# Kernel optimization log

Measured on AMD Instinct MI355X. Metric: run time of the kernel, lower is better.

Reference implementation:

```python
import jax, jax.numpy as jnp
import numpy as np

B, S, HIDDEN = 1, 2048, 2048
NUM_HEADS, MLA_DIM = 16, 128
HEAD_DIM = HIDDEN // NUM_HEADS
ROPE_BASE = 10000.0


def setup_inputs() -> dict:
    key = jax.random.key(0)
    ks = jax.random.split(key, 5)
    sd = 0.02
    hidden_states = jax.random.normal(ks[0], (B, S, HIDDEN), dtype=jnp.float32)
    wq = jax.random.normal(ks[1], (HIDDEN, NUM_HEADS * MLA_DIM), dtype=jnp.float32) * sd
    wk = jax.random.normal(ks[2], (HIDDEN, NUM_HEADS * MLA_DIM), dtype=jnp.float32) * sd
    wv = jax.random.normal(ks[3], (HIDDEN, HIDDEN), dtype=jnp.float32) * sd
    wo = jax.random.normal(ks[4], (HIDDEN, HIDDEN), dtype=jnp.float32) * sd
    # causal additive mask [B, 1, S, S]
    causal = jnp.tril(jnp.ones((S, S), dtype=bool))
    attention_mask = jnp.where(causal, 0.0, -1e9).astype(jnp.float32)[None, None]
    attention_mask = jnp.broadcast_to(attention_mask, (B, 1, S, S))
    return {"hidden_states": hidden_states, "wq": wq, "wk": wk, "wv": wv,
            "wo": wo, "attention_mask": attention_mask}


def _rope_cos_sin(seq_len, dim, dtype):
    inv_freq = 1.0 / (ROPE_BASE ** (jnp.arange(0, dim, 2, dtype=jnp.float32) / dim))
    t = jnp.arange(seq_len, dtype=jnp.float32)
    freqs = jnp.einsum('i,j->ij', t, inv_freq)           # [S, dim/2]
    emb = jnp.concatenate([freqs, freqs], axis=-1)       # [S, dim]
    cos = jnp.cos(emb)[None, :, None, :].astype(dtype)   # [1, S, 1, dim]
    sin = jnp.sin(emb)[None, :, None, :].astype(dtype)
    return cos, sin


def _rotate_half(x):
    x1, x2 = jnp.split(x, 2, axis=-1)
    return jnp.concatenate([-x2, x1], axis=-1)


def reference(hidden_states, wq, wk, wv, wo, attention_mask):
    b, s, _ = hidden_states.shape
    q = (hidden_states @ wq).reshape(b, s, NUM_HEADS, MLA_DIM)
    k = (hidden_states @ wk).reshape(b, s, NUM_HEADS, MLA_DIM)
    v = (hidden_states @ wv).reshape(b, s, NUM_HEADS, HEAD_DIM)
    cos, sin = _rope_cos_sin(s, MLA_DIM, q.dtype)
    q = q * cos + _rotate_half(q) * sin
    k = k * cos + _rotate_half(k) * sin
    scale = 1.0 / np.sqrt(MLA_DIM)
    scores = jnp.einsum('bqhd,bkhd->bhqk', q, k) * scale + attention_mask
    probs = jax.nn.softmax(scores, axis=-1)
    out = jnp.einsum('bhqk,bkhd->bqhd', probs, v).reshape(b, s, HIDDEN)
    return out @ wo
```

## Files before the change

### kernel.cpp

```cpp
#include <hip/hip_runtime.h>
#include <math.h>

namespace {

constexpr int SEQ = 2048;
constexpr int HID = 2048;
constexpr int NH  = 16;
constexpr int DH  = 128;

using f32x4  = __attribute__((ext_vector_type(4))) float;
using short8 = __attribute__((ext_vector_type(8))) short;

__device__ __forceinline__ unsigned short f2bf(float f) {
    unsigned u = __float_as_uint(f);
    u += 0x7FFFu + ((u >> 16) & 1u);
    return (unsigned short)(u >> 16);
}

typedef const __attribute__((address_space(1))) unsigned int GUI;
typedef __attribute__((address_space(3))) unsigned int LUI;
__device__ __forceinline__ void async16(const void* g, void* l) {
    __builtin_amdgcn_global_load_lds((GUI*)g, (LUI*)l, 16, 0, 0);
}

__global__ __launch_bounds__(256)
void cast_bf16(const float* __restrict__ X, unsigned short* __restrict__ Y)
{
    const int i = blockIdx.x * 256 + threadIdx.x;
    const float4 v = reinterpret_cast<const float4*>(X)[i];
    ushort4 o;
    o.x = f2bf(v.x); o.y = f2bf(v.y); o.z = f2bf(v.z); o.w = f2bf(v.w);
    reinterpret_cast<ushort4*>(Y)[i] = o;
}

__global__ __launch_bounds__(256)
void transpose_cast3(const float* __restrict__ w0, const float* __restrict__ w1,
                     const float* __restrict__ w2, unsigned short* __restrict__ WT3)
{
    const int z = blockIdx.z;
    const float* W = (z == 0) ? w0 : (z == 1) ? w1 : w2;
    unsigned short* WT = WT3 + (size_t)z * HID * HID;

    __shared__ float t[32][33];
    const int tx = threadIdx.x & 31, ty = threadIdx.x >> 5;
    const int n0 = blockIdx.x * 32, k0 = blockIdx.y * 32;
    #pragma unroll
    for (int i = 0; i < 4; ++i)
        t[ty + 8 * i][tx] = W[(size_t)(k0 + ty + 8 * i) * HID + n0 + tx];
    __syncthreads();
    #pragma unroll
    for (int i = 0; i < 4; ++i)
        WT[(size_t)(n0 + ty + 8 * i) * HID + k0 + tx] = f2bf(t[tx][ty + 8 * i]);
}

__global__ __launch_bounds__(256)
void transpose_cast(const float* __restrict__ W, unsigned short* __restrict__ WT)
{
    __shared__ float t[32][33];
    const int tx = threadIdx.x & 31, ty = threadIdx.x >> 5;
    const int n0 = blockIdx.x * 32, k0 = blockIdx.y * 32;
    #pragma unroll
    for (int i = 0; i < 4; ++i)
        t[ty + 8 * i][tx] = W[(size_t)(k0 + ty + 8 * i) * HID + n0 + tx];
    __syncthreads();
    #pragma unroll
    for (int i = 0; i < 4; ++i)
        WT[(size_t)(n0 + ty + 8 * i) * HID + k0 + tx] = f2bf(t[tx][ty + 8 * i]);
}

__global__ __launch_bounds__(256)
void transp_bf16(const unsigned short* __restrict__ X, unsigned short* __restrict__ Y)
{
    __shared__ unsigned short t[32][34];
    const int tx = threadIdx.x & 31, ty = threadIdx.x >> 5;
    const int i0 = blockIdx.y * 32, j0 = blockIdx.x * 32;
    #pragma unroll
    for (int q = 0; q < 4; ++q)
        t[ty + 8 * q][tx] = X[(size_t)(i0 + ty + 8 * q) * HID + j0 + tx];
    __syncthreads();
    #pragma unroll
    for (int q = 0; q < 4; ++q)
        Y[(size_t)(j0 + ty + 8 * q) * HID + i0 + tx] = t[tx][ty + 8 * q];
}

__global__ __launch_bounds__(256)
void gemm_qkv(const unsigned short* __restrict__ A,
              const unsigned short* __restrict__ Bt3,
              unsigned short* __restrict__ Qo,
              unsigned short* __restrict__ Ko,
              unsigned short* __restrict__ Vo)
{
    __shared__ unsigned short As[128 * 32];
    __shared__ unsigned short Bs[128 * 32];

    const int tid  = threadIdx.x;
    const int lane = tid & 63;
    const int w    = tid >> 6;
    const int wr   = w >> 1, wc = w & 1;

    const int b  = blockIdx.x;
    const int sw = (b & 7) * 96 + (b >> 3);
    const int mt = sw & 15, nt = sw >> 4;
    const int m0  = mt * 128;
    const int n0g = nt * 128;
    const int wi  = nt >> 4;
    const int n0  = (nt & 15) * 128;
    unsigned short* C = (wi == 0) ? Qo : (wi == 1) ? Ko : Vo;

    const int srow = lane >> 2;
    const int scol = (lane & 3) * 8;
    const int c0   = w * 2;

    const unsigned short* gA = A   + (size_t)(m0  + c0 * 16 + srow) * HID + scol;
    const unsigned short* gB = Bt3 + (size_t)(n0g + c0 * 16 + srow) * HID + scol;
    unsigned short* lA = &As[c0 * 16 * 32];
    unsigned short* lB = &Bs[c0 * 16 * 32];

    f32x4 acc[4][4] = {};

    for (int k0 = 0; k0 < HID; k0 += 32) {
        __syncthreads();
        async16(gA + k0,            lA);
        async16(gA + 16 * HID + k0, lA + 16 * 32);
        async16(gB + k0,            lB);
        async16(gB + 16 * HID + k0, lB + 16 * 32);
        __syncthreads();

        short8 af[4], bf[4];
        const int kb = (lane >> 4) * 8;
        #pragma unroll
        for (int i = 0; i < 4; ++i) {
            af[i] = *reinterpret_cast<const short8*>(
                &As[(wr * 64 + i * 16 + (lane & 15)) * 32 + kb]);
            bf[i] = *reinterpret_cast<const short8*>(
                &Bs[(wc * 64 + i * 16 + (lane & 15)) * 32 + kb]);
        }
        #pragma unroll
        for (int i = 0; i < 4; ++i)
            #pragma unroll
            for (int j = 0; j < 4; ++j)
                acc[i][j] = __builtin_amdgcn_mfma_f32_16x16x32_bf16(
                    af[i], bf[j], acc[i][j], 0, 0, 0);
    }

    const int cl = lane & 15, rg = (lane >> 4) * 4;
    #pragma unroll
    for (int i = 0; i < 4; ++i)
        #pragma unroll
        for (int j = 0; j < 4; ++j)
            #pragma unroll
            for (int rr = 0; rr < 4; ++rr) {
                const int row = m0 + wr * 64 + i * 16 + rg + rr;
                const int col = n0 + wc * 64 + j * 16 + cl;
                C[(size_t)row * HID + col] = f2bf(acc[i][j][rr]);
            }
}

__global__ __launch_bounds__(256)
void gemm_wo(const unsigned short* __restrict__ A,
             const unsigned short* __restrict__ Bt,
             float* __restrict__ C)
{
    __shared__ unsigned short As[128 * 32];
    __shared__ unsigned short Bs[128 * 32];

    const int tid  = threadIdx.x;
    const int lane = tid & 63;
    const int w    = tid >> 6;
    const int wr   = w >> 1, wc = w & 1;

    const int b  = blockIdx.x;
    const int sw = (b & 7) * 32 + (b >> 3);
    const int m0 = (sw >> 4) * 128, n0 = (sw & 15) * 128;

    const int srow = lane >> 2;
    const int scol = (lane & 3) * 8;
    const int c0   = w * 2;

    const unsigned short* gA = A  + (size_t)(m0 + c0 * 16 + srow) * HID + scol;
    const unsigned short* gB = Bt + (size_t)(n0 + c0 * 16 + srow) * HID + scol;
    unsigned short* lA = &As[c0 * 16 * 32];
    unsigned short* lB = &Bs[c0 * 16 * 32];

    f32x4 acc[4][4] = {};

    for (int k0 = 0; k0 < HID; k0 += 32) {
        __syncthreads();
        async16(gA + k0,            lA);
        async16(gA + 16 * HID + k0, lA + 16 * 32);
        async16(gB + k0,            lB);
        async16(gB + 16 * HID + k0, lB + 16 * 32);
        __syncthreads();

        short8 af[4], bf[4];
        const int kb = (lane >> 4) * 8;
        #pragma unroll
        for (int i = 0; i < 4; ++i) {
            af[i] = *reinterpret_cast<const short8*>(
                &As[(wr * 64 + i * 16 + (lane & 15)) * 32 + kb]);
            bf[i] = *reinterpret_cast<const short8*>(
                &Bs[(wc * 64 + i * 16 + (lane & 15)) * 32 + kb]);
        }
        #pragma unroll
        for (int i = 0; i < 4; ++i)
            #pragma unroll
            for (int j = 0; j < 4; ++j)
                acc[i][j] = __builtin_amdgcn_mfma_f32_16x16x32_bf16(
                    af[i], bf[j], acc[i][j], 0, 0, 0);
    }

    const int cl = lane & 15, rg = (lane >> 4) * 4;
    #pragma unroll
    for (int i = 0; i < 4; ++i)
        #pragma unroll
        for (int j = 0; j < 4; ++j)
            #pragma unroll
            for (int rr = 0; rr < 4; ++rr) {
                const int row = m0 + wr * 64 + i * 16 + rg + rr;
                const int col = n0 + wc * 64 + j * 16 + cl;
                C[(size_t)row * HID + col] = acc[i][j][rr];
            }
}

__global__ __launch_bounds__(256)
void rope_qk(unsigned short* __restrict__ Q, unsigned short* __restrict__ K)
{
    const int idx = blockIdx.x * 256 + threadIdx.x;
    const int d = idx & 63;
    const int h = (idx >> 6) & (NH - 1);
    const int s = idx >> 10;

    const float invf = exp2f(-(float)d * (13.287712379549449f / 64.0f));
    float sn, c;
    sincosf((float)s * invf, &sn, &c);

    const float SC = 0.08838834764831845f;
    const size_t base = (size_t)s * HID + h * DH + d;

    const float a0 = __uint_as_float((unsigned)Q[base]      << 16);
    const float a1 = __uint_as_float((unsigned)Q[base + 64] << 16);
    Q[base]      = f2bf((a0 * c - a1 * sn) * SC);
    Q[base + 64] = f2bf((a1 * c + a0 * sn) * SC);
    const float b0 = __uint_as_float((unsigned)K[base]      << 16);
    const float b1 = __uint_as_float((unsigned)K[base + 64] << 16);
    K[base]      = f2bf(b0 * c - b1 * sn);
    K[base + 64] = f2bf(b1 * c + b0 * sn);
}

__global__ __launch_bounds__(256)
void attn_mfma(const unsigned short* __restrict__ Q,
               const unsigned short* __restrict__ K,
               const unsigned short* __restrict__ Vt,
               unsigned short* __restrict__ AO)
{
    __shared__ unsigned short Ks[64 * 128];
    __shared__ unsigned short Vs[128 * 64];
    __shared__ unsigned short Ps[4][16 * 72];

    const int tid  = threadIdx.x;
    const int lane = tid & 63;
    const int w    = tid >> 6;

    const int b  = blockIdx.x;
    const int i_ = b & 31;
    const int h  = b >> 5;
    const int qb = (b < 256) ? i_ : 31 - i_;
    const int q0 = qb * 64;

    const int cl = lane & 15;
    const int lg = lane >> 4;
    const int rg = lg * 4;

    short8 aq[4];
    const unsigned short* qrow = Q + (size_t)(q0 + w * 16 + cl) * HID + h * DH;
    #pragma unroll
    for (int c = 0; c < 4; ++c)
        aq[c] = *reinterpret_cast<const short8*>(qrow + c * 32 + lg * 8);

    f32x4 o[8] = {};
    float m[4] = {-INFINITY, -INFINITY, -INFINITY, -INFINITY};
    float l[4] = {};

    const int nt = qb + 1;
    for (int t = 0; t < nt; ++t) {
        const int k0 = t * 64;

        __syncthreads();
        #pragma unroll
        for (int i = 0; i < 4; ++i) {
            const int rb = i * 16 + w * 4;
            const int r  = rb + lg;
            const int gs = cl ^ (r & 7);
            async16(K + (size_t)(k0 + r) * HID + h * DH + gs * 8, &Ks[rb * 128]);
        }
        #pragma unroll
        for (int i = 0; i < 4; ++i) {
            const int rb = i * 32 + w * 8;
            const int r  = rb + (lane >> 3);
            const int gs = (lane & 7) ^ (r & 7);
            async16(Vt + (size_t)(h * DH + r) * SEQ + k0 + gs * 8, &Vs[rb * 64]);
        }
        __syncthreads();

        f32x4 s4[4] = {};
        #pragma unroll
        for (int jk = 0; jk < 4; ++jk) {
            #pragma unroll
            for (int c = 0; c < 4; ++c) {
                const int row  = jk * 16 + cl;
                const int slot = (c * 4 + lg) ^ (row & 7);
                const short8 bk = *reinterpret_cast<const short8*>(
                    &Ks[row * 128 + slot * 8]);
                s4[jk] = __builtin_amdgcn_mfma_f32_16x16x32_bf16(
                    aq[c], bk, s4[jk], 0, 0, 0);
            }
        }

        if (t == nt - 1) {
            #pragma unroll
            for (int jk = 0; jk < 4; ++jk)
                #pragma unroll
                for (int r = 0; r < 4; ++r)
                    if (jk * 16 + cl > w * 16 + rg + r)
                        s4[jk][r] = -INFINITY;
        }

        float corr[4], rs[4];
        #pragma unroll
        for (int r = 0; r < 4; ++r) {
            float mx = fmaxf(fmaxf(s4[0][r], s4[1][r]),
                             fmaxf(s4[2][r], s4[3][r]));
            #pragma unroll
            for (int off = 1; off < 16; off <<= 1)
                mx = fmaxf(mx, __shfl_xor(mx, off, 64));
            const float mn = fmaxf(m[r], mx);
            corr[r] = __expf(m[r] - mn);
            m[r] = mn;
            rs[r] = 0.0f;
        }
        #pragma unroll
        for (int jk = 0; jk < 4; ++jk)
            #pragma unroll
            for (int r = 0; r < 4; ++r) {
                const float p = __expf(s4[jk][r] - m[r]);
                Ps[w][(rg + r) * 72 + jk * 16 + cl] = f2bf(p);
                rs[r] += p;
            }
        #pragma unroll
        for (int r = 0; r < 4; ++r) {
            #pragma unroll
            for (int off = 1; off < 16; off <<= 1)
                rs[r] += __shfl_xor(rs[r], off, 64);
            l[r] = l[r] * corr[r] + rs[r];
        }
        #pragma unroll
        for (int jd = 0; jd < 8; ++jd)
            #pragma unroll
            for (int r = 0; r < 4; ++r)
                o[jd][r] *= corr[r];

        #pragma unroll
        for (int c = 0; c < 2; ++c) {
            const short8 pa = *reinterpret_cast<const short8*>(
                &Ps[w][cl * 72 + c * 32 + lg * 8]);
            #pragma unroll
            for (int jd = 0; jd < 8; ++jd) {
                const int row  = jd * 16 + cl;
                const int slot = (c * 4 + lg) ^ (row & 7);
                const short8 bv = *reinterpret_cast<const short8*>(
                    &Vs[row * 64 + slot * 8]);
                o[jd] = __builtin_amdgcn_mfma_f32_16x16x32_bf16(
                    pa, bv, o[jd], 0, 0, 0);
            }
        }
    }

    #pragma unroll
    for (int r = 0; r < 4; ++r) {
        const float inv = 1.0f / l[r];
        unsigned short* orow = AO + (size_t)(q0 + w * 16 + rg + r) * HID + h * DH;
        #pragma unroll
        for (int jd = 0; jd < 8; ++jd)
            orow[jd * 16 + cl] = f2bf(o[jd][r] * inv);
    }
}

}

extern "C" void kernel_launch(void* const* d_in, const int* in_sizes, int n_in,
                              void* d_out, int out_size, void* d_ws, size_t ws_size,
                              hipStream_t stream)
{
    (void)in_sizes; (void)n_in; (void)out_size; (void)ws_size;

    const float* hs = (const float*)d_in[0];
    const float* wq = (const float*)d_in[1];
    const float* wk = (const float*)d_in[2];
    const float* wv = (const float*)d_in[3];
    const float* wo = (const float*)d_in[4];
    float* out = (float*)d_out;

    const size_t NE = (size_t)SEQ * HID;
    unsigned short* hsb = (unsigned short*)d_ws;
    unsigned short* Qb  = hsb + NE;
    unsigned short* Kb  = Qb + NE;
    unsigned short* Vb  = Kb + NE;
    unsigned short* WT3 = Vb + NE;
    unsigned short* AOb = WT3 + NE;
    unsigned short* WTo = WT3;
    unsigned short* Vt  = hsb;

    const dim3 tgrid(HID / 32, HID / 32);

    cast_bf16<<<(NE / 4) / 256, 256, 0, stream>>>(hs, hsb);

    transpose_cast3<<<dim3(HID / 32, HID / 32, 3), 256, 0, stream>>>(wq, wk, wv, WT3);

    gemm_qkv<<<768, 256, 0, stream>>>(hsb, WT3, Qb, Kb, Vb);

    rope_qk<<<(SEQ * NH * 64) / 256, 256, 0, stream>>>(Qb, Kb);

    transp_bf16<<<tgrid, 256, 0, stream>>>(Vb, Vt);

    attn_mfma<<<512, 256, 0, stream>>>(Qb, Kb, Vt, AOb);

    transpose_cast<<<tgrid, 256, 0, stream>>>(wo, WTo);
    gemm_wo<<<256, 256, 0, stream>>>(AOb, WTo, out);
}
```

Measured before the change: 319.6 us.

## Double-buffer attention K/V tiles, split-K the output GEMM, widen weight transposes

The attention kernel now double-buffers its K and V shared-memory tiles, so the next tile's async loads are issued while the current tile is computed, with one barrier per iteration. The output projection GEMM is split into two K-halves across 512 blocks, writing partial sums into reused workspace that a new reduce kernel adds together. This targets the GPU being under-filled when there was only one block per tile. The weight transpose-cast kernels now handle 64-column tiles with float2 loads. The costs are double the attention LDS footprint, an extra fp32 read/write pass plus a launch for the reduction, and reliance on workspace aliasing being safe.

```diff
diff --git a/kernel.cpp b/kernel.cpp
--- a/kernel.cpp
+++ b/kernel.cpp
@@ -41,31 +41,45 @@
     const float* W = (z == 0) ? w0 : (z == 1) ? w1 : w2;
     unsigned short* WT = WT3 + (size_t)z * HID * HID;
 
-    __shared__ float t[32][33];
+    __shared__ float t[32][66];
     const int tx = threadIdx.x & 31, ty = threadIdx.x >> 5;
-    const int n0 = blockIdx.x * 32, k0 = blockIdx.y * 32;
-    #pragma unroll
-    for (int i = 0; i < 4; ++i)
-        t[ty + 8 * i][tx] = W[(size_t)(k0 + ty + 8 * i) * HID + n0 + tx];
+    const int n0 = blockIdx.x * 64, k0 = blockIdx.y * 32;
+    #pragma unroll
+    for (int i = 0; i < 4; ++i) {
+        const int kr = ty + 8 * i;
+        const float2 v = *reinterpret_cast<const float2*>(
+            &W[(size_t)(k0 + kr) * HID + n0 + 2 * tx]);
+        t[kr][2 * tx]     = v.x;
+        t[kr][2 * tx + 1] = v.y;
+    }
     __syncthreads();
     #pragma unroll
-    for (int i = 0; i < 4; ++i)
-        WT[(size_t)(n0 + ty + 8 * i) * HID + k0 + tx] = f2bf(t[tx][ty + 8 * i]);
+    for (int i = 0; i < 8; ++i) {
+        const int n = ty + 8 * i;
+        WT[(size_t)(n0 + n) * HID + k0 + tx] = f2bf(t[tx][n]);
+    }
 }
 
 __global__ __launch_bounds__(256)
 void transpose_cast(const float* __restrict__ W, unsigned short* __restrict__ WT)
 {
-    __shared__ float t[32][33];
+    __shared__ float t[32][66];
     const int tx = threadIdx.x & 31, ty = threadIdx.x >> 5;
-    const int n0 = blockIdx.x * 32, k0 = blockIdx.y * 32;
-    #pragma unroll
-    for (int i = 0; i < 4; ++i)
-        t[ty + 8 * i][tx] = W[(size_t)(k0 + ty + 8 * i) * HID + n0 + tx];
+    const int n0 = blockIdx.x * 64, k0 = blockIdx.y * 32;
+    #pragma unroll
+    for (int i = 0; i < 4; ++i) {
+        const int kr = ty + 8 * i;
+        const float2 v = *reinterpret_cast<const float2*>(
+            &W[(size_t)(k0 + kr) * HID + n0 + 2 * tx]);
+        t[kr][2 * tx]     = v.x;
+        t[kr][2 * tx + 1] = v.y;
+    }
     __syncthreads();
     #pragma unroll
-    for (int i = 0; i < 4; ++i)
-        WT[(size_t)(n0 + ty + 8 * i) * HID + k0 + tx] = f2bf(t[tx][ty + 8 * i]);
+    for (int i = 0; i < 8; ++i) {
+        const int n = ty + 8 * i;
+        WT[(size_t)(n0 + n) * HID + k0 + tx] = f2bf(t[tx][n]);
+    }
 }
 
 __global__ __launch_bounds__(256)
@@ -157,9 +171,9 @@
 }
 
 __global__ __launch_bounds__(256)
-void gemm_wo(const unsigned short* __restrict__ A,
-             const unsigned short* __restrict__ Bt,
-             float* __restrict__ C)
+void gemm_wo_sk(const unsigned short* __restrict__ A,
+                const unsigned short* __restrict__ Bt,
+                float* __restrict__ P0, float* __restrict__ P1)
 {
     __shared__ unsigned short As[128 * 32];
     __shared__ unsigned short Bs[128 * 32];
@@ -169,22 +183,26 @@
     const int w    = tid >> 6;
     const int wr   = w >> 1, wc = w & 1;
 
-    const int b  = blockIdx.x;
-    const int sw = (b & 7) * 32 + (b >> 3);
+    const int b     = blockIdx.x;
+    const int chunk = b >> 8;
+    const int bb    = b & 255;
+    const int sw = (bb & 7) * 32 + (bb >> 3);
     const int m0 = (sw >> 4) * 128, n0 = (sw & 15) * 128;
+    float* C = chunk ? P1 : P0;
+    const int kbase = chunk * 1024;
 
     const int srow = lane >> 2;
     const int scol = (lane & 3) * 8;
     const int c0   = w * 2;
 
-    const unsigned short* gA = A  + (size_t)(m0 + c0 * 16 + srow) * HID + scol;
-    const unsigned short* gB = Bt + (size_t)(n0 + c0 * 16 + srow) * HID + scol;
+    const unsigned short* gA = A  + (size_t)(m0 + c0 * 16 + srow) * HID + kbase + scol;
+    const unsigned short* gB = Bt + (size_t)(n0 + c0 * 16 + srow) * HID + kbase + scol;
     unsigned short* lA = &As[c0 * 16 * 32];
     unsigned short* lB = &Bs[c0 * 16 * 32];
 
     f32x4 acc[4][4] = {};
 
-    for (int k0 = 0; k0 < HID; k0 += 32) {
+    for (int k0 = 0; k0 < 1024; k0 += 32) {
         __syncthreads();
         async16(gA + k0,            lA);
         async16(gA + 16 * HID + k0, lA + 16 * 32);
@@ -220,6 +238,17 @@
                 const int col = n0 + wc * 64 + j * 16 + cl;
                 C[(size_t)row * HID + col] = acc[i][j][rr];
             }
+}
+
+__global__ __launch_bounds__(256)
+void reduce2(const float* __restrict__ P0, const float* __restrict__ P1,
+             float* __restrict__ out)
+{
+    const int i = blockIdx.x * 256 + threadIdx.x;
+    const float4 a = reinterpret_cast<const float4*>(P0)[i];
+    const float4 b = reinterpret_cast<const float4*>(P1)[i];
+    float4 r; r.x = a.x + b.x; r.y = a.y + b.y; r.z = a.z + b.z; r.w = a.w + b.w;
+    reinterpret_cast<float4*>(out)[i] = r;
 }
 
 __global__ __launch_bounds__(256)
@@ -253,8 +282,8 @@
                const unsigned short* __restrict__ Vt,
                unsigned short* __restrict__ AO)
 {
-    __shared__ unsigned short Ks[64 * 128];
-    __shared__ unsigned short Vs[128 * 64];
+    __shared__ unsigned short Ks[2][64 * 128];
+    __shared__ unsigned short Vs[2][128 * 64];
     __shared__ unsigned short Ps[4][16 * 72];
 
     const int tid  = threadIdx.x;
@@ -281,26 +310,33 @@
     float m[4] = {-INFINITY, -INFINITY, -INFINITY, -INFINITY};
     float l[4] = {};
 
-    const int nt = qb + 1;
-    for (int t = 0; t < nt; ++t) {
+    auto stage = [&](int t, int buf) {
         const int k0 = t * 64;
-
-        __syncthreads();
         #pragma unroll
         for (int i = 0; i < 4; ++i) {
             const int rb = i * 16 + w * 4;
             const int r  = rb + lg;
             const int gs = cl ^ (r & 7);
-            async16(K + (size_t)(k0 + r) * HID + h * DH + gs * 8, &Ks[rb * 128]);
+            async16(K + (size_t)(k0 + r) * HID + h * DH + gs * 8,
+                    &Ks[buf][rb * 128]);
         }
         #pragma unroll
         for (int i = 0; i < 4; ++i) {
             const int rb = i * 32 + w * 8;
             const int r  = rb + (lane >> 3);
             const int gs = (lane & 7) ^ (r & 7);
-            async16(Vt + (size_t)(h * DH + r) * SEQ + k0 + gs * 8, &Vs[rb * 64]);
-        }
+            async16(Vt + (size_t)(h * DH + r) * SEQ + k0 + gs * 8,
+                    &Vs[buf][rb * 64]);
+        }
+    };
+
+    const int nt = qb + 1;
+    stage(0, 0);
+
+    for (int t = 0; t < nt; ++t) {
+        const int cur = t & 1;
         __syncthreads();
+        if (t + 1 < nt) stage(t + 1, cur ^ 1);
 
         f32x4 s4[4] = {};
         #pragma unroll
@@ -310,7 +346,7 @@
                 const int row  = jk * 16 + cl;
                 const int slot = (c * 4 + lg) ^ (row & 7);
                 const short8 bk = *reinterpret_cast<const short8*>(
-                    &Ks[row * 128 + slot * 8]);
+                    &Ks[cur][row * 128 + slot * 8]);
                 s4[jk] = __builtin_amdgcn_mfma_f32_16x16x32_bf16(
                     aq[c], bk, s4[jk], 0, 0, 0);
             }
@@ -368,7 +404,7 @@
                 const int row  = jd * 16 + cl;
                 const int slot = (c * 4 + lg) ^ (row & 7);
                 const short8 bv = *reinterpret_cast<const short8*>(
-                    &Vs[row * 64 + slot * 8]);
+                    &Vs[cur][row * 64 + slot * 8]);
                 o[jd] = __builtin_amdgcn_mfma_f32_16x16x32_bf16(
                     pa, bv, o[jd], 0, 0, 0);
             }
@@ -409,21 +445,22 @@
     unsigned short* AOb = WT3 + NE;
     unsigned short* WTo = WT3;
     unsigned short* Vt  = hsb;
-
-    const dim3 tgrid(HID / 32, HID / 32);
+    float* P0 = (float*)hsb;
+    float* P1 = (float*)Kb;
 
     cast_bf16<<<(NE / 4) / 256, 256, 0, stream>>>(hs, hsb);
 
-    transpose_cast3<<<dim3(HID / 32, HID / 32, 3), 256, 0, stream>>>(wq, wk, wv, WT3);
+    transpose_cast3<<<dim3(HID / 64, HID / 32, 3), 256, 0, stream>>>(wq, wk, wv, WT3);
 
     gemm_qkv<<<768, 256, 0, stream>>>(hsb, WT3, Qb, Kb, Vb);
 
     rope_qk<<<(SEQ * NH * 64) / 256, 256, 0, stream>>>(Qb, Kb);
 
-    transp_bf16<<<tgrid, 256, 0, stream>>>(Vb, Vt);
+    transp_bf16<<<dim3(HID / 32, HID / 32), 256, 0, stream>>>(Vb, Vt);
 
     attn_mfma<<<512, 256, 0, stream>>>(Qb, Kb, Vt, AOb);
 
-    transpose_cast<<<tgrid, 256, 0, stream>>>(wo, WTo);
-    gemm_wo<<<256, 256, 0, stream>>>(AOb, WTo, out);
-}
+    transpose_cast<<<dim3(HID / 64, HID / 32), 256, 0, stream>>>(wo, WTo);
+    gemm_wo_sk<<<512, 256, 0, stream>>>(AOb, WTo, P0, P1);
+    reduce2<<<(int)(NE / 4 / 256), 256, 0, stream>>>(P0, P1, out);
+}
```

Measured after the change: 313.1 us. -2.0%, faster.
